# Kernel optimization log

Hardware: AMD Instinct MI355X
Metric: run time of the kernel (lower is better)

## Reference

```python
import jax, jax.numpy as jnp
import numpy as np

N = 50000      # nodes
E = 640000     # edges
FIN = 100      # raw node feature dim (nn.Linear(100, d_model))
D = 128        # d_model (dim_hidden)
H = 8          # num_heads
DH = D // H    # head dim
L = 4          # num_layers
DFF = 4 * D    # dim_feedforward
G = 64         # number of graphs in the batch
SCALE = DH ** -0.5


def setup_inputs() -> dict:
    key = jax.random.key(0)
    ks = jax.random.split(key, 12)
    x = jax.random.normal(ks[0], (N, FIN), jnp.float32)
    edge_index = jax.random.randint(ks[1], (2, E), 0, N, dtype=jnp.int64)
    batch = jnp.sort(jax.random.randint(ks[2], (N,), 0, G, dtype=jnp.int64))

    def w(k, shape, fan_in):
        return jax.random.normal(k, shape, jnp.float32) * (fan_in ** -0.5)

    W_embed = w(ks[3], (FIN, D), FIN)          # embedding, bias=False
    Wqk = w(ks[4], (L, D, 2 * D), D)           # to_qk, bias=False
    Wv = w(ks[5], (L, D, D), D)                # to_v, bias=False
    Wout = w(ks[6], (L, D, D), D)              # out_proj
    b_out = jnp.zeros((L, D), jnp.float32)
    W1 = w(ks[7], (L, D, DFF), D)              # FFN linear1
    b1 = jnp.zeros((L, DFF), jnp.float32)
    W2 = w(ks[8], (L, DFF, D), DFF)            # FFN linear2
    b2 = jnp.zeros((L, D), jnp.float32)
    return dict(x=x, edge_index=edge_index, batch=batch, W_embed=W_embed,
                Wqk=Wqk, Wv=Wv, Wout=Wout, b_out=b_out, W1=W1, b1=b1,
                W2=W2, b2=b2)


def reference(x, edge_index, batch, W_embed, Wqk, Wv, Wout, b_out, W1, b1, W2, b2):
    src = edge_index[0]  # j (message source)
    dst = edge_index[1]  # i (aggregation target)
    h = x @ W_embed  # [N, D]; dropout is identity at eval
    for l in range(L):
        # --- DAG multi-head attention (PyG MessagePassing, aggr='add') ---
        qk = h @ Wqk[l]
        q, k = qk[:, :D], qk[:, D:]
        v = h @ Wv[l]
        qj = q[src].reshape(E, H, DH)   # qk_j: gathered at source
        ki = k[dst].reshape(E, H, DH)   # qk_i: gathered at target
        logits = (qj * ki).sum(-1) * SCALE  # [E, H]
        # segment softmax over edges sharing the same target node
        m = jax.ops.segment_max(logits, dst, num_segments=N)        # [N, H]
        p = jnp.exp(logits - m[dst])
        ssum = jax.ops.segment_sum(p, dst, num_segments=N)          # [N, H]
        attn = p / ssum[dst]
        msg = (v[src].reshape(E, H, DH) * attn[:, :, None]).reshape(E, D)
        agg = jax.ops.segment_sum(msg, dst, num_segments=N)         # [N, D]
        h = h + (agg @ Wout[l] + b_out[l])   # residual; norm1 = Identity
        # --- FFN (relu) ---
        ff = jax.nn.relu(h @ W1[l] + b1[l]) @ W2[l] + b2[l]
        h = h + ff                            # residual; norm2 = Identity
    # global mean pool over graphs
    cnt = jax.ops.segment_sum(jnp.ones((N,), h.dtype), batch, num_segments=G)
    pooled = jax.ops.segment_sum(h, batch, num_segments=G) / jnp.maximum(cnt, 1.0)[:, None]
    return pooled
```

## Files before the change

### kernel.cpp

```cpp
#include <hip/hip_runtime.h>
#include <hip/hip_bf16.h>
#include <math.h>

#define D 128
#define NH 8
#define DFF 512
#define NG 64
#define NL 4
#define FIN 100
#define SCALE 0.25f
#define QKV 384

typedef __attribute__((ext_vector_type(8))) short short8;
typedef __attribute__((ext_vector_type(4))) float f32x4;

__global__ void count_kernel(const int* __restrict__ dst, int* __restrict__ cnt, int E) {
    int e = blockIdx.x * 256 + threadIdx.x;
    if (e < E) atomicAdd(&cnt[dst[e]], 1);
}

__global__ __launch_bounds__(1024) void scan_block_kernel(const int* __restrict__ cnt,
        int* __restrict__ incl, int* __restrict__ partials, int n) {
    __shared__ int s[1024];
    int tid = threadIdx.x;
    int gid = blockIdx.x * 1024 + tid;
    int val = (gid < n) ? cnt[gid] : 0;
    s[tid] = val;
    __syncthreads();
    for (int o = 1; o < 1024; o <<= 1) {
        int t = (tid >= o) ? s[tid - o] : 0;
        __syncthreads();
        s[tid] += t;
        __syncthreads();
    }
    if (gid < n) incl[gid] = s[tid];
    if (tid == 1023) partials[blockIdx.x] = s[1023];
}

__global__ void scan_partials_kernel(int* __restrict__ partials, int nb) {
    if (threadIdx.x == 0 && blockIdx.x == 0) {
        int run = 0;
        for (int i = 0; i < nb; ++i) { int t = partials[i]; partials[i] = run; run += t; }
    }
}

__global__ void finalize_off_kernel(const int* __restrict__ cnt, const int* __restrict__ incl,
        const int* __restrict__ partials, int* __restrict__ off, int* __restrict__ cur,
        int n, int E) {
    int gid = blockIdx.x * 256 + threadIdx.x;
    if (gid < n) {
        int v = incl[gid] - cnt[gid] + partials[gid >> 10];
        off[gid] = v;
        cur[gid] = v;
    }
    if (gid == 0) off[n] = E;
}

__global__ void scatter_kernel(const int* __restrict__ src, const int* __restrict__ dst,
        int* __restrict__ cur, int* __restrict__ csr_src, int E) {
    int e = blockIdx.x * 256 + threadIdx.x;
    if (e < E) {
        int p = atomicAdd(&cur[dst[e]], 1);
        csr_src[p] = src[e];
    }
}

__global__ void transpose_cvt_kernel(const float* __restrict__ W, __hip_bfloat16* __restrict__ Bt,
        int K, int N, int ldl) {
    int l = blockIdx.y;
    const float* w = W + (size_t)l * K * N;
    __hip_bfloat16* bt = Bt + (size_t)l * ldl;
    int idx = blockIdx.x * 256 + threadIdx.x;
    if (idx >= K * N) return;
    int n = idx / K, k = idx - n * K;
    bt[(size_t)n * K + k] = __float2bfloat16(w[(size_t)k * N + n]);
}

__global__ void pad_cvt_x_kernel(const float* __restrict__ x, __hip_bfloat16* __restrict__ xb, int n) {
    int idx = blockIdx.x * 256 + threadIdx.x;
    if (idx >= n * 128) return;
    int r = idx >> 7, c = idx & 127;
    xb[idx] = (c < FIN) ? __float2bfloat16(x[(size_t)r * FIN + c]) : __float2bfloat16(0.f);
}

__global__ void wembT_kernel(const float* __restrict__ W, __hip_bfloat16* __restrict__ Bt) {
    int idx = blockIdx.x * 256 + threadIdx.x;
    if (idx >= 128 * 128) return;
    int n = idx >> 7, k = idx & 127;
    Bt[idx] = (k < FIN) ? __float2bfloat16(W[(size_t)k * 128 + n]) : __float2bfloat16(0.f);
}

template<int EPI>
__global__ __launch_bounds__(256) void gemm_mfma(
        const __hip_bfloat16* __restrict__ A, const __hip_bfloat16* __restrict__ Bt,
        const float* __restrict__ bias,
        float* __restrict__ Cf, __hip_bfloat16* __restrict__ Cb,
        int M, int N, int K) {
    __shared__ __align__(16) unsigned short As[128][64];
    __shared__ __align__(16) unsigned short Bs[64][64];
    int t = threadIdx.x;
    int wave = t >> 6, lane = t & 63;
    int row0 = blockIdx.x * 128, col0 = blockIdx.y * 64;
    f32x4 acc[2][4] = {};

    int sr = t >> 3;
    int sc = t & 7;

    for (int k0 = 0; k0 < K; k0 += 64) {
#pragma unroll
        for (int i = 0; i < 4; ++i) {
            int r = i * 32 + sr;
            int gr = row0 + r;
            if (gr >= M) gr = M - 1;
            *reinterpret_cast<short8*>(&As[r][(sc ^ (r & 7)) << 3]) =
                *reinterpret_cast<const short8*>(&A[(size_t)gr * K + k0 + (sc << 3)]);
        }
#pragma unroll
        for (int i = 0; i < 2; ++i) {
            int r = i * 32 + sr;
            *reinterpret_cast<short8*>(&Bs[r][(sc ^ (r & 7)) << 3]) =
                *reinterpret_cast<const short8*>(&Bt[(size_t)(col0 + r) * K + k0 + (sc << 3)]);
        }
        __syncthreads();
#pragma unroll
        for (int kk = 0; kk < 64; kk += 32) {
            int lr = lane & 15;
            int kc = (kk >> 3) + (lane >> 4);
            short8 a[2], b[4];
#pragma unroll
            for (int m = 0; m < 2; ++m) {
                int r = wave * 32 + m * 16 + lr;
                a[m] = *reinterpret_cast<const short8*>(&As[r][(kc ^ (r & 7)) << 3]);
            }
#pragma unroll
            for (int n = 0; n < 4; ++n) {
                int r = n * 16 + lr;
                b[n] = *reinterpret_cast<const short8*>(&Bs[r][(kc ^ (r & 7)) << 3]);
            }
#pragma unroll
            for (int m = 0; m < 2; ++m)
#pragma unroll
                for (int n = 0; n < 4; ++n)
                    acc[m][n] = __builtin_amdgcn_mfma_f32_16x16x32_bf16(a[m], b[n], acc[m][n], 0, 0, 0);
        }
        __syncthreads();
    }

    int lr = lane & 15, rg = (lane >> 4) * 4;
#pragma unroll
    for (int m = 0; m < 2; ++m) {
#pragma unroll
        for (int n = 0; n < 4; ++n) {
            int col = col0 + n * 16 + lr;
#pragma unroll
            for (int j = 0; j < 4; ++j) {
                int row = row0 + wave * 32 + m * 16 + rg + j;
                if (row < M) {
                    float val = acc[m][n][j];
                    if (EPI == 0) {
                        Cb[(size_t)row * N + col] = __float2bfloat16(val);
                    } else if (EPI == 1) {
                        val = fmaxf(val + bias[col], 0.f);
                        Cb[(size_t)row * N + col] = __float2bfloat16(val);
                    } else if (EPI == 2) {
                        val += bias[col] + Cf[(size_t)row * N + col];
                        Cf[(size_t)row * N + col] = val;
                        Cb[(size_t)row * N + col] = __float2bfloat16(val);
                    } else {
                        Cf[(size_t)row * N + col] = val;
                        Cb[(size_t)row * N + col] = __float2bfloat16(val);
                    }
                }
            }
        }
    }
}

__global__ __launch_bounds__(256) void attn_kernel(const __hip_bfloat16* __restrict__ qkvb,
        const int* __restrict__ off, const int* __restrict__ csr_src,
        __hip_bfloat16* __restrict__ aggb, int n) {
    int wave = threadIdx.x >> 6;
    int lane = threadIdx.x & 63;
    int i = blockIdx.x * 4 + wave;
    if (i >= n) return;
    const unsigned* qv = reinterpret_cast<const unsigned*>(qkvb);
    unsigned ku = qv[(size_t)i * 192 + 64 + lane];
    float kx = __uint_as_float(ku << 16);
    float ky = __uint_as_float(ku & 0xffff0000u);
    int e0 = off[i], e1 = off[i + 1];
    float m = -INFINITY, ssum = 0.f, ax = 0.f, ay = 0.f;
    int e = e0;
    for (; e + 4 <= e1; e += 4) {
        int s0 = csr_src[e], s1 = csr_src[e + 1], s2 = csr_src[e + 2], s3 = csr_src[e + 3];
        unsigned q0 = qv[(size_t)s0 * 192 + lane];
        unsigned q1 = qv[(size_t)s1 * 192 + lane];
        unsigned q2 = qv[(size_t)s2 * 192 + lane];
        unsigned q3 = qv[(size_t)s3 * 192 + lane];
        unsigned w0 = qv[(size_t)s0 * 192 + 128 + lane];
        unsigned w1 = qv[(size_t)s1 * 192 + 128 + lane];
        unsigned w2 = qv[(size_t)s2 * 192 + 128 + lane];
        unsigned w3 = qv[(size_t)s3 * 192 + 128 + lane];
        float l0 = __uint_as_float(q0 << 16) * kx + __uint_as_float(q0 & 0xffff0000u) * ky;
        float l1 = __uint_as_float(q1 << 16) * kx + __uint_as_float(q1 & 0xffff0000u) * ky;
        float l2 = __uint_as_float(q2 << 16) * kx + __uint_as_float(q2 & 0xffff0000u) * ky;
        float l3 = __uint_as_float(q3 << 16) * kx + __uint_as_float(q3 & 0xffff0000u) * ky;
        l0 += __shfl_xor(l0, 1); l1 += __shfl_xor(l1, 1); l2 += __shfl_xor(l2, 1); l3 += __shfl_xor(l3, 1);
        l0 += __shfl_xor(l0, 2); l1 += __shfl_xor(l1, 2); l2 += __shfl_xor(l2, 2); l3 += __shfl_xor(l3, 2);
        l0 += __shfl_xor(l0, 4); l1 += __shfl_xor(l1, 4); l2 += __shfl_xor(l2, 4); l3 += __shfl_xor(l3, 4);
        l0 *= SCALE; l1 *= SCALE; l2 *= SCALE; l3 *= SCALE;
        float mx = fmaxf(fmaxf(l0, l1), fmaxf(l2, l3));
        float mn = fmaxf(m, mx);
        float corr = __expf(m - mn);
        float p0 = __expf(l0 - mn);
        float p1 = __expf(l1 - mn);
        float p2 = __expf(l2 - mn);
        float p3 = __expf(l3 - mn);
        ssum = ssum * corr + ((p0 + p1) + (p2 + p3));
        ax = ax * corr + p0 * __uint_as_float(w0 << 16) + p1 * __uint_as_float(w1 << 16)
                       + p2 * __uint_as_float(w2 << 16) + p3 * __uint_as_float(w3 << 16);
        ay = ay * corr + p0 * __uint_as_float(w0 & 0xffff0000u) + p1 * __uint_as_float(w1 & 0xffff0000u)
                       + p2 * __uint_as_float(w2 & 0xffff0000u) + p3 * __uint_as_float(w3 & 0xffff0000u);
        m = mn;
    }
    for (; e < e1; ++e) {
        int s0 = csr_src[e];
        unsigned q0 = qv[(size_t)s0 * 192 + lane];
        unsigned w0 = qv[(size_t)s0 * 192 + 128 + lane];
        float l0 = __uint_as_float(q0 << 16) * kx + __uint_as_float(q0 & 0xffff0000u) * ky;
        l0 += __shfl_xor(l0, 1); l0 += __shfl_xor(l0, 2); l0 += __shfl_xor(l0, 4);
        l0 *= SCALE;
        float mn = fmaxf(m, l0);
        float corr = __expf(m - mn);
        float pe = __expf(l0 - mn);
        ssum = ssum * corr + pe;
        ax = ax * corr + pe * __uint_as_float(w0 << 16);
        ay = ay * corr + pe * __uint_as_float(w0 & 0xffff0000u);
        m = mn;
    }
    float inv = (ssum > 0.f) ? 1.f / ssum : 0.f;
    __hip_bfloat162 o;
    o.x = __float2bfloat16(ax * inv);
    o.y = __float2bfloat16(ay * inv);
    *reinterpret_cast<__hip_bfloat162*>(aggb + (size_t)i * 128 + lane * 2) = o;
}

__global__ void group_bounds_kernel(const int* __restrict__ batch, int n, int* __restrict__ gstart) {
    int g = threadIdx.x;
    if (g > NG) return;
    int lo = 0, hi = n;
    while (lo < hi) {
        int mid = (lo + hi) >> 1;
        if (batch[mid] < g) lo = mid + 1; else hi = mid;
    }
    gstart[g] = lo;
}

__global__ __launch_bounds__(256) void pool_stage1(const float* __restrict__ h,
        const int* __restrict__ gstart, float* __restrict__ pws) {
    int g = blockIdx.x, sub = blockIdx.y;
    int s = gstart[g], e = gstart[g + 1];
    int c = threadIdx.x & 127;
    int half = threadIdx.x >> 7;
    float acc = 0.f;
    for (int r = s + sub * 2 + half; r < e; r += 16)
        acc += h[(size_t)r * 128 + c];
    __shared__ float tmp[2][128];
    tmp[half][c] = acc;
    __syncthreads();
    if (half == 0)
        pws[((size_t)g * 8 + sub) * 128 + c] = tmp[0][c] + tmp[1][c];
}

__global__ void pool_stage2(const float* __restrict__ pws, const int* __restrict__ gstart,
        float* __restrict__ out) {
    int g = blockIdx.x, c = threadIdx.x;
    float s = 0.f;
#pragma unroll
    for (int i = 0; i < 8; ++i) s += pws[((size_t)g * 8 + i) * 128 + c];
    float cntf = (float)(gstart[g + 1] - gstart[g]);
    out[(size_t)g * 128 + c] = s / fmaxf(cntf, 1.f);
}

extern "C" void kernel_launch(void* const* d_in, const int* in_sizes, int n_in,
                              void* d_out, int out_size, void* d_ws, size_t ws_size,
                              hipStream_t stream) {
    const float* x = (const float*)d_in[0];
    const int* ei = (const int*)d_in[1];
    const int* batch = (const int*)d_in[2];
    const float* W_embed = (const float*)d_in[3];
    const float* Wqk = (const float*)d_in[4];
    const float* Wv = (const float*)d_in[5];
    const float* Wout = (const float*)d_in[6];
    const float* b_out = (const float*)d_in[7];
    const float* W1 = (const float*)d_in[8];
    const float* b1 = (const float*)d_in[9];
    const float* W2 = (const float*)d_in[10];
    const float* b2 = (const float*)d_in[11];

    int Nn = in_sizes[2];
    int E = in_sizes[1] / 2;

    char* p = (char*)d_ws;
    auto alloc = [&](size_t bytes) {
        char* r = p;
        p += (bytes + 255) & ~(size_t)255;
        return r;
    };
    float* h32 = (float*)alloc((size_t)Nn * D * 4);
    __hip_bfloat16* hb = (__hip_bfloat16*)alloc((size_t)Nn * D * 2);
    __hip_bfloat16* aggb = (__hip_bfloat16*)alloc((size_t)Nn * D * 2);
    char* uni = alloc((size_t)Nn * DFF * 2);
    __hip_bfloat16* qkvb = (__hip_bfloat16*)uni;
    __hip_bfloat16* ff1b = (__hip_bfloat16*)uni;
    __hip_bfloat16* xb = (__hip_bfloat16*)alloc((size_t)Nn * D * 2);
    __hip_bfloat16* WembT = (__hip_bfloat16*)alloc((size_t)D * D * 2);
    __hip_bfloat16* WqkvT = (__hip_bfloat16*)alloc((size_t)NL * QKV * D * 2);
    __hip_bfloat16* WoutT = (__hip_bfloat16*)alloc((size_t)NL * D * D * 2);
    __hip_bfloat16* W1T = (__hip_bfloat16*)alloc((size_t)NL * D * DFF * 2);
    __hip_bfloat16* W2T = (__hip_bfloat16*)alloc((size_t)NL * DFF * D * 2);
    int* csr_src = (int*)alloc((size_t)E * 4);
    int* cnt = (int*)alloc((size_t)Nn * 4);
    int* incl = (int*)alloc((size_t)Nn * 4);
    int* off = (int*)alloc(((size_t)Nn + 1) * 4);
    int* cur = (int*)alloc((size_t)Nn * 4);
    int* partials = (int*)alloc(1024 * 4);
    int* gstart = (int*)alloc((NG + 1) * 4);
    float* pws = (float*)alloc((size_t)NG * 8 * 128 * 4);

    const int* e_src = ei;
    const int* e_dst = ei + E;

    hipMemsetAsync(cnt, 0, (size_t)Nn * 4, stream);
    count_kernel<<<(E + 255) / 256, 256, 0, stream>>>(e_dst, cnt, E);
    int nsb = (Nn + 1023) / 1024;
    scan_block_kernel<<<nsb, 1024, 0, stream>>>(cnt, incl, partials, Nn);
    scan_partials_kernel<<<1, 64, 0, stream>>>(partials, nsb);
    finalize_off_kernel<<<(Nn + 255) / 256, 256, 0, stream>>>(cnt, incl, partials, off, cur, Nn, E);
    scatter_kernel<<<(E + 255) / 256, 256, 0, stream>>>(e_src, e_dst, cur, csr_src, E);

    transpose_cvt_kernel<<<dim3((2 * D * D + 255) / 256, NL), 256, 0, stream>>>(
        Wqk, WqkvT, D, 2 * D, QKV * D);
    transpose_cvt_kernel<<<dim3((D * D + 255) / 256, NL), 256, 0, stream>>>(
        Wv, WqkvT + (size_t)2 * D * D, D, D, QKV * D);
    transpose_cvt_kernel<<<dim3((D * D + 255) / 256, NL), 256, 0, stream>>>(
        Wout, WoutT, D, D, D * D);
    transpose_cvt_kernel<<<dim3((D * DFF + 255) / 256, NL), 256, 0, stream>>>(
        W1, W1T, D, DFF, D * DFF);
    transpose_cvt_kernel<<<dim3((DFF * D + 255) / 256, NL), 256, 0, stream>>>(
        W2, W2T, DFF, D, DFF * D);
    wembT_kernel<<<(128 * 128 + 255) / 256, 256, 0, stream>>>(W_embed, WembT);
    pad_cvt_x_kernel<<<((size_t)Nn * 128 + 255) / 256, 256, 0, stream>>>(x, xb, Nn);

    int gmb = (Nn + 127) / 128;
    gemm_mfma<3><<<dim3(gmb, D / 64), 256, 0, stream>>>(
        xb, WembT, nullptr, h32, hb, Nn, D, D);

    for (int l = 0; l < NL; ++l) {
        gemm_mfma<0><<<dim3(gmb, QKV / 64), 256, 0, stream>>>(
            hb, WqkvT + (size_t)l * QKV * D, nullptr, nullptr, qkvb, Nn, QKV, D);
        attn_kernel<<<(Nn + 3) / 4, 256, 0, stream>>>(qkvb, off, csr_src, aggb, Nn);
        gemm_mfma<2><<<dim3(gmb, D / 64), 256, 0, stream>>>(
            aggb, WoutT + (size_t)l * D * D, b_out + (size_t)l * D, h32, hb, Nn, D, D);
        gemm_mfma<1><<<dim3(gmb, DFF / 64), 256, 0, stream>>>(
            hb, W1T + (size_t)l * D * DFF, b1 + (size_t)l * DFF, nullptr, ff1b, Nn, DFF, D);
        gemm_mfma<2><<<dim3(gmb, D / 64), 256, 0, stream>>>(
            ff1b, W2T + (size_t)l * DFF * D, b2 + (size_t)l * D, h32, hb, Nn, D, DFF);
    }

    group_bounds_kernel<<<1, 128, 0, stream>>>(batch, Nn, gstart);
    pool_stage1<<<dim3(NG, 8), 256, 0, stream>>>(h32, gstart, pws);
    pool_stage2<<<NG, 128, 0, stream>>>(pws, gstart, (float*)d_out);
}
```

Baseline: 765.8 us.

## Fuse out-projection, residual and FFN into one per-row-tile kernel

Replaces three GEMM launches per layer (out-proj with residual, FFN linear1 with relu, FFN linear2 with residual) with one kernel. Each block owns 128 rows, keeps the updated h tile in LDS and streams W1/W2 in 64-wide chunks, so the [N,512] ff1 intermediate never goes to global memory. This removes the ff1 write and read traffic and two launches. In exchange it uses 80KB of LDS per block, which limits occupancy, grids only about 391 blocks, and serialises each chunk's loads and compute behind barriers.

```diff
diff --git a/kernel.cpp b/kernel.cpp
--- a/kernel.cpp
+++ b/kernel.cpp
@@ -13,6 +13,11 @@
 
 typedef __attribute__((ext_vector_type(8))) short short8;
 typedef __attribute__((ext_vector_type(4))) float f32x4;
+
+__device__ inline unsigned short f2bf(float v) {
+    __hip_bfloat16 b = __float2bfloat16(v);
+    return *reinterpret_cast<unsigned short*>(&b);
+}
 
 __global__ void count_kernel(const int* __restrict__ dst, int* __restrict__ cnt, int E) {
     int e = blockIdx.x * 256 + threadIdx.x;
@@ -159,17 +164,174 @@
                     float val = acc[m][n][j];
                     if (EPI == 0) {
                         Cb[(size_t)row * N + col] = __float2bfloat16(val);
-                    } else if (EPI == 1) {
-                        val = fmaxf(val + bias[col], 0.f);
-                        Cb[(size_t)row * N + col] = __float2bfloat16(val);
-                    } else if (EPI == 2) {
-                        val += bias[col] + Cf[(size_t)row * N + col];
-                        Cf[(size_t)row * N + col] = val;
-                        Cb[(size_t)row * N + col] = __float2bfloat16(val);
                     } else {
                         Cf[(size_t)row * N + col] = val;
                         Cb[(size_t)row * N + col] = __float2bfloat16(val);
                     }
+                }
+            }
+        }
+    }
+}
+
+__global__ __launch_bounds__(256) void fused_out_ffn(
+        const __hip_bfloat16* __restrict__ aggb, const __hip_bfloat16* __restrict__ WoutT,
+        const float* __restrict__ b_out,
+        const __hip_bfloat16* __restrict__ W1T, const float* __restrict__ b1,
+        const __hip_bfloat16* __restrict__ W2T, const float* __restrict__ b2,
+        float* __restrict__ h32, __hip_bfloat16* __restrict__ hb, int M) {
+    extern __shared__ __align__(16) unsigned short smem[];
+    unsigned short* As  = smem;
+    unsigned short* Bs  = smem + 16384;
+    unsigned short* W1s = Bs;
+    unsigned short* ff1s = Bs + 8192;
+    unsigned short* W2s = smem + 32768;
+
+    int t = threadIdx.x;
+    int wave = t >> 6, lane = t & 63;
+    int lr = lane & 15, lg = lane >> 4;
+    int row0 = blockIdx.x * 128;
+
+#pragma unroll
+    for (int i = 0; i < 8; ++i) {
+        int idx = t + i * 256;
+        int r = idx >> 4, ch = idx & 15;
+        int gr = row0 + r; if (gr >= M) gr = M - 1;
+        *reinterpret_cast<short8*>(&As[r * 128 + ((ch ^ (r & 7)) << 3)]) =
+            *reinterpret_cast<const short8*>(&aggb[(size_t)gr * 128 + ch * 8]);
+        *reinterpret_cast<short8*>(&Bs[r * 128 + ((ch ^ (r & 7)) << 3)]) =
+            *reinterpret_cast<const short8*>(&WoutT[(size_t)r * 128 + ch * 8]);
+    }
+    __syncthreads();
+
+    f32x4 acc1[2][8] = {};
+#pragma unroll
+    for (int kk4 = 0; kk4 < 4; ++kk4) {
+        int kc = kk4 * 4 + lg;
+        short8 a[2], b[8];
+#pragma unroll
+        for (int m = 0; m < 2; ++m) {
+            int r = wave * 32 + m * 16 + lr;
+            a[m] = *reinterpret_cast<const short8*>(&As[r * 128 + ((kc ^ (r & 7)) << 3)]);
+        }
+#pragma unroll
+        for (int n = 0; n < 8; ++n) {
+            int r = n * 16 + lr;
+            b[n] = *reinterpret_cast<const short8*>(&Bs[r * 128 + ((kc ^ (r & 7)) << 3)]);
+        }
+#pragma unroll
+        for (int m = 0; m < 2; ++m)
+#pragma unroll
+            for (int n = 0; n < 8; ++n)
+                acc1[m][n] = __builtin_amdgcn_mfma_f32_16x16x32_bf16(a[m], b[n], acc1[m][n], 0, 0, 0);
+    }
+
+#pragma unroll
+    for (int m = 0; m < 2; ++m) {
+#pragma unroll
+        for (int n = 0; n < 8; ++n) {
+            int col = n * 16 + lr;
+            float bo = b_out[col];
+#pragma unroll
+            for (int j = 0; j < 4; ++j) {
+                int rl = wave * 32 + m * 16 + lg * 4 + j;
+                int row = row0 + rl;
+                float hv = (row < M) ? h32[(size_t)row * 128 + col] : 0.f;
+                float val = acc1[m][n][j] + bo + hv;
+                if (row < M) h32[(size_t)row * 128 + col] = val;
+                As[rl * 128 + (((col >> 3) ^ (rl & 7)) << 3) + (col & 7)] = f2bf(val);
+            }
+        }
+    }
+
+    f32x4 h2acc[2][8] = {};
+    for (int c = 0; c < 8; ++c) {
+        __syncthreads();
+#pragma unroll
+        for (int i = 0; i < 4; ++i) {
+            int idx = t + i * 256;
+            int r = idx >> 4, ch = idx & 15;
+            *reinterpret_cast<short8*>(&W1s[r * 128 + ((ch ^ (r & 7)) << 3)]) =
+                *reinterpret_cast<const short8*>(&W1T[((size_t)(c * 64 + r)) * 128 + ch * 8]);
+        }
+#pragma unroll
+        for (int i = 0; i < 4; ++i) {
+            int idx = t + i * 256;
+            int r = idx >> 3, ch = idx & 7;
+            *reinterpret_cast<short8*>(&W2s[r * 64 + ((ch ^ (r & 7)) << 3)]) =
+                *reinterpret_cast<const short8*>(&W2T[(size_t)r * 512 + c * 64 + ch * 8]);
+        }
+        __syncthreads();
+        f32x4 acc2[2][4] = {};
+#pragma unroll
+        for (int kk4 = 0; kk4 < 4; ++kk4) {
+            int kc = kk4 * 4 + lg;
+            short8 a[2], b[4];
+#pragma unroll
+            for (int m = 0; m < 2; ++m) {
+                int r = wave * 32 + m * 16 + lr;
+                a[m] = *reinterpret_cast<const short8*>(&As[r * 128 + ((kc ^ (r & 7)) << 3)]);
+            }
+#pragma unroll
+            for (int n = 0; n < 4; ++n) {
+                int r = n * 16 + lr;
+                b[n] = *reinterpret_cast<const short8*>(&W1s[r * 128 + ((kc ^ (r & 7)) << 3)]);
+            }
+#pragma unroll
+            for (int m = 0; m < 2; ++m)
+#pragma unroll
+                for (int n = 0; n < 4; ++n)
+                    acc2[m][n] = __builtin_amdgcn_mfma_f32_16x16x32_bf16(a[m], b[n], acc2[m][n], 0, 0, 0);
+        }
+#pragma unroll
+        for (int m = 0; m < 2; ++m) {
+#pragma unroll
+            for (int n = 0; n < 4; ++n) {
+                int col = n * 16 + lr;
+                float bb = b1[c * 64 + col];
+#pragma unroll
+                for (int j = 0; j < 4; ++j) {
+                    int rl = wave * 32 + m * 16 + lg * 4 + j;
+                    float val = fmaxf(acc2[m][n][j] + bb, 0.f);
+                    ff1s[rl * 64 + (((col >> 3) ^ (rl & 7)) << 3) + (col & 7)] = f2bf(val);
+                }
+            }
+        }
+#pragma unroll
+        for (int kk4 = 0; kk4 < 2; ++kk4) {
+            int kc = kk4 * 4 + lg;
+            short8 a[2], b[8];
+#pragma unroll
+            for (int m = 0; m < 2; ++m) {
+                int r = wave * 32 + m * 16 + lr;
+                a[m] = *reinterpret_cast<const short8*>(&ff1s[r * 64 + ((kc ^ (r & 7)) << 3)]);
+            }
+#pragma unroll
+            for (int n = 0; n < 8; ++n) {
+                int r = n * 16 + lr;
+                b[n] = *reinterpret_cast<const short8*>(&W2s[r * 64 + ((kc ^ (r & 7)) << 3)]);
+            }
+#pragma unroll
+            for (int m = 0; m < 2; ++m)
+#pragma unroll
+                for (int n = 0; n < 8; ++n)
+                    h2acc[m][n] = __builtin_amdgcn_mfma_f32_16x16x32_bf16(a[m], b[n], h2acc[m][n], 0, 0, 0);
+        }
+    }
+
+#pragma unroll
+    for (int m = 0; m < 2; ++m) {
+#pragma unroll
+        for (int n = 0; n < 8; ++n) {
+            int col = n * 16 + lr;
+            float bb = b2[col];
+#pragma unroll
+            for (int j = 0; j < 4; ++j) {
+                int row = row0 + wave * 32 + m * 16 + lg * 4 + j;
+                if (row < M) {
+                    float val = h2acc[m][n][j] + bb + h32[(size_t)row * 128 + col];
+                    h32[(size_t)row * 128 + col] = val;
+                    hb[(size_t)row * 128 + col] = __float2bfloat16(val);
                 }
             }
         }
@@ -309,9 +471,7 @@
     float* h32 = (float*)alloc((size_t)Nn * D * 4);
     __hip_bfloat16* hb = (__hip_bfloat16*)alloc((size_t)Nn * D * 2);
     __hip_bfloat16* aggb = (__hip_bfloat16*)alloc((size_t)Nn * D * 2);
-    char* uni = alloc((size_t)Nn * DFF * 2);
-    __hip_bfloat16* qkvb = (__hip_bfloat16*)uni;
-    __hip_bfloat16* ff1b = (__hip_bfloat16*)uni;
+    __hip_bfloat16* qkvb = (__hip_bfloat16*)alloc((size_t)Nn * QKV * 2);
     __hip_bfloat16* xb = (__hip_bfloat16*)alloc((size_t)Nn * D * 2);
     __hip_bfloat16* WembT = (__hip_bfloat16*)alloc((size_t)D * D * 2);
     __hip_bfloat16* WqkvT = (__hip_bfloat16*)alloc((size_t)NL * QKV * D * 2);
@@ -355,16 +515,17 @@
     gemm_mfma<3><<<dim3(gmb, D / 64), 256, 0, stream>>>(
         xb, WembT, nullptr, h32, hb, Nn, D, D);
 
+    size_t fused_lds = (size_t)(16384 + 16384 + 8192) * sizeof(unsigned short);
+
     for (int l = 0; l < NL; ++l) {
         gemm_mfma<0><<<dim3(gmb, QKV / 64), 256, 0, stream>>>(
             hb, WqkvT + (size_t)l * QKV * D, nullptr, nullptr, qkvb, Nn, QKV, D);
         attn_kernel<<<(Nn + 3) / 4, 256, 0, stream>>>(qkvb, off, csr_src, aggb, Nn);
-        gemm_mfma<2><<<dim3(gmb, D / 64), 256, 0, stream>>>(
-            aggb, WoutT + (size_t)l * D * D, b_out + (size_t)l * D, h32, hb, Nn, D, D);
-        gemm_mfma<1><<<dim3(gmb, DFF / 64), 256, 0, stream>>>(
-            hb, W1T + (size_t)l * D * DFF, b1 + (size_t)l * DFF, nullptr, ff1b, Nn, DFF, D);
-        gemm_mfma<2><<<dim3(gmb, D / 64), 256, 0, stream>>>(
-            ff1b, W2T + (size_t)l * DFF * D, b2 + (size_t)l * D, h32, hb, Nn, D, DFF);
+        fused_out_ffn<<<gmb, 256, fused_lds, stream>>>(
+            aggb, WoutT + (size_t)l * D * D, b_out + (size_t)l * D,
+            W1T + (size_t)l * D * DFF, b1 + (size_t)l * DFF,
+            W2T + (size_t)l * DFF * D, b2 + (size_t)l * D,
+            h32, hb, Nn);
     }
 
     group_bounds_kernel<<<1, 128, 0, stream>>>(batch, Nn, gstart);
```

New measurement: 664.2 us. 13.3% less time.
